# Kernel tuning notes

Hardware: AMD Instinct MI355X
Metric: run time of the kernel (lower is better)

The kernel has to match this reference:

```python
import jax, jax.numpy as jnp
import numpy as np

N = 100_000   # nodes
E = 1_600_000 # edges (avg degree 16)
D = 128       # in_dim
H = 128       # hidden_dim


def _glorot(key, shape):
    s = 1.0 / np.sqrt(shape[0])
    return jax.random.uniform(key, shape, jnp.float32, -s, s)


def setup_inputs() -> dict:
    key = jax.random.key(0)
    ks = jax.random.split(key, 8)
    x = jax.random.normal(ks[0], (N, D), jnp.float32)
    edge_index = jax.random.randint(ks[1], (2, E), 0, N)
    return {
        "x": x,
        "edge_index": edge_index,
        "Wn0": _glorot(ks[2], (D, H)),
        "Wr0": _glorot(ks[3], (D, H)),
        "b0": jnp.zeros((H,), jnp.float32),
        "Wn1": _glorot(ks[4], (H, H)),
        "Wr1": _glorot(ks[5], (H, H)),
        "b1": jnp.zeros((H,), jnp.float32),
        "Wh": _glorot(ks[6], (H, 1)),
        "bh": jnp.zeros((1,), jnp.float32),
    }


def _mean_agg(h, src, dst, n):
    # mean of source-node features scattered onto destination nodes
    summed = jax.ops.segment_sum(h[src], dst, num_segments=n)  # [N, F]
    cnt = jax.ops.segment_sum(jnp.ones((src.shape[0],), h.dtype), dst,
                              num_segments=n)
    return summed / jnp.maximum(cnt, 1.0)[:, None]


def _sage_layer(h, src, dst, Wn, Wr, b):
    # PyG SAGEConv (mean aggr): lin_l(mean_neighbors) + lin_r(root) + bias
    agg = _mean_agg(h, src, dst, h.shape[0])
    return agg @ Wn + h @ Wr + b


def reference(x, edge_index, Wn0, Wr0, b0, Wn1, Wr1, b1, Wh, bh):
    src, dst = edge_index[0], edge_index[1]
    h = jax.nn.relu(_sage_layer(x, src, dst, Wn0, Wr0, b0))  # dropout = identity (eval)
    h = jax.nn.relu(_sage_layer(h, src, dst, Wn1, Wr1, b1))
    logits = (h @ Wh + bh)[:, 0]  # squeeze(-1) -> [N]
    return logits
```

## Files before the change

### kernel.cpp

```cpp
#include <hip/hip_runtime.h>

#define THREADS 256
#define SCAN_ITEMS 8
#define NSB 256
#define BKT_MAX 3200
#define CHUNK 1024

typedef float f32x4 __attribute__((ext_vector_type(4)));
typedef __bf16 bf16x8 __attribute__((ext_vector_type(8)));
typedef int intx4 __attribute__((ext_vector_type(4)));

__device__ inline unsigned short f32_to_bf16_rne(float f) {
    unsigned int u = __float_as_uint(f);
    unsigned int r = u + 0x7fffu + ((u >> 16) & 1u);
    return (unsigned short)(r >> 16);
}
__device__ inline float bf16_bits_to_f32(unsigned short h) {
    return __uint_as_float(((unsigned int)h) << 16);
}
__device__ inline uint4 pack8(const unsigned short* s) {
    uint4 u;
    u.x = (unsigned int)s[0] | ((unsigned int)s[1] << 16);
    u.y = (unsigned int)s[2] | ((unsigned int)s[3] << 16);
    u.z = (unsigned int)s[4] | ((unsigned int)s[5] << 16);
    u.w = (unsigned int)s[6] | ((unsigned int)s[7] << 16);
    return u;
}

__global__ __launch_bounds__(256) void hist32(const int* __restrict__ dst,
                                              int* __restrict__ hist,
                                              int E, int nbkt, int chunk) {
    __shared__ int lh[BKT_MAX];
    const int tid = threadIdx.x, blk = blockIdx.x;
    for (int i = tid; i < nbkt; i += 256) lh[i] = 0;
    __syncthreads();
    int s = blk * chunk, e = s + chunk; if (e > E) e = E;
    if (((size_t)dst & 15) == 0) {
        int n4 = (e > s) ? ((e - s) >> 2) : 0;
        const intx4* d4p = (const intx4*)(dst + s);
        for (int i = tid; i < n4; i += 256) {
            intx4 d4 = d4p[i];
#pragma unroll
            for (int k = 0; k < 4; k++) atomicAdd(&lh[d4[k] >> 5], 1);
        }
        for (int j = s + (n4 << 2) + tid; j < e; j += 256) atomicAdd(&lh[dst[j] >> 5], 1);
    } else {
        for (int j = s + tid; j < e; j += 256) atomicAdd(&lh[dst[j] >> 5], 1);
    }
    __syncthreads();
    for (int i = tid; i < nbkt; i += 256) hist[i * NSB + blk] = lh[i];
}

__global__ void scan1_kernel(const int* __restrict__ cnt, int* __restrict__ off,
                             int* __restrict__ bsums, int n) {
    __shared__ int sdata[THREADS];
    int base = blockIdx.x * (THREADS * SCAN_ITEMS) + threadIdx.x * SCAN_ITEMS;
    int vals[SCAN_ITEMS];
    int tsum = 0;
#pragma unroll
    for (int k = 0; k < SCAN_ITEMS; k++) {
        int idx = base + k;
        int v = (idx < n) ? cnt[idx] : 0;
        vals[k] = tsum;
        tsum += v;
    }
    sdata[threadIdx.x] = tsum;
    __syncthreads();
    for (int s = 1; s < THREADS; s <<= 1) {
        int y = (threadIdx.x >= (unsigned)s) ? sdata[threadIdx.x - s] : 0;
        __syncthreads();
        sdata[threadIdx.x] += y;
        __syncthreads();
    }
    int texcl = sdata[threadIdx.x] - tsum;
#pragma unroll
    for (int k = 0; k < SCAN_ITEMS; k++) {
        int idx = base + k;
        if (idx < n) off[idx] = texcl + vals[k];
    }
    if (threadIdx.x == THREADS - 1) bsums[blockIdx.x] = sdata[THREADS - 1];
}

__global__ void scan2_wave(const int* __restrict__ bsums, int* __restrict__ bbase,
                           int nb, int* __restrict__ offN) {
    const int lane = threadIdx.x;
    int carry = 0;
    for (int base = 0; base < nb; base += 64) {
        int i = base + lane;
        int v = (i < nb) ? bsums[i] : 0;
        int x = v;
#pragma unroll
        for (int s = 1; s < 64; s <<= 1) {
            int y = __shfl_up(x, s);
            if (lane >= s) x += y;
        }
        if (i < nb) bbase[i] = carry + x - v;
        carry += __shfl(x, 63);
    }
    if (lane == 0) *offN = carry;
}

__global__ void scan3b_kernel(int* __restrict__ off, const int* __restrict__ bbase, int n) {
    int i = blockIdx.x * blockDim.x + threadIdx.x;
    if (i < n) off[i] += bbase[i >> 11];
}

__global__ __launch_bounds__(256) void scatter32(const int* __restrict__ src,
                                                 const int* __restrict__ dst,
                                                 const int* __restrict__ hstS,
                                                 int* __restrict__ esrt,
                                                 int E, int nbkt, int chunk) {
    __shared__ int cur[BKT_MAX];
    const int tid = threadIdx.x, blk = blockIdx.x;
    for (int i = tid; i < nbkt; i += 256) cur[i] = hstS[i * NSB + blk];
    __syncthreads();
    int s = blk * chunk, e = s + chunk; if (e > E) e = E;
    if ((((size_t)dst | (size_t)src) & 15) == 0) {
        int n4 = (e > s) ? ((e - s) >> 2) : 0;
        const intx4* d4p = (const intx4*)(dst + s);
        const intx4* s4p = (const intx4*)(src + s);
        for (int i = tid; i < n4; i += 256) {
            intx4 d4 = d4p[i];
            intx4 s4 = s4p[i];
#pragma unroll
            for (int k = 0; k < 4; k++) {
                int d = d4[k];
                int p = atomicAdd(&cur[d >> 5], 1);
                esrt[p] = s4[k] | ((d & 31) << 17);
            }
        }
        for (int j = s + (n4 << 2) + tid; j < e; j += 256) {
            int d = dst[j];
            int p = atomicAdd(&cur[d >> 5], 1);
            esrt[p] = src[j] | ((d & 31) << 17);
        }
    } else {
        for (int j = s + tid; j < e; j += 256) {
            int d = dst[j];
            int p = atomicAdd(&cur[d >> 5], 1);
            esrt[p] = src[j] | ((d & 31) << 17);
        }
    }
}

__global__ void cvt_bf16_kernel(const float4* __restrict__ x, ushort4* __restrict__ o, int n4) {
    int i = blockIdx.x * blockDim.x + threadIdx.x;
    if (i < n4) {
        float4 v = x[i];
        ushort4 r;
        r.x = f32_to_bf16_rne(v.x);
        r.y = f32_to_bf16_rne(v.y);
        r.z = f32_to_bf16_rne(v.z);
        r.w = f32_to_bf16_rne(v.w);
        o[i] = r;
    }
}

__global__ void swizzle_w_kernel(const float* __restrict__ Wn, const float* __restrict__ Wr,
                                 uint4* __restrict__ out) {
    int id = blockIdx.x * blockDim.x + threadIdx.x;
    if (id >= 4096) return;
    int lane = id & 63;
    int nt = (id >> 6) & 7;
    int t = id >> 9;
    int kbase = t * 32 + (lane >> 4) * 8;
    int col = nt * 16 + (lane & 15);
    unsigned short hi[8], lo[8];
#pragma unroll
    for (int j = 0; j < 8; j++) {
        int k = kbase + j;
        const float* W = (k < 128) ? (Wn + (size_t)k * 128) : (Wr + (size_t)(k - 128) * 128);
        float v = W[col];
        unsigned short h = f32_to_bf16_rne(v);
        hi[j] = h;
        lo[j] = f32_to_bf16_rne(v - bf16_bits_to_f32(h));
    }
    out[(size_t)((t * 8 + nt) * 2 + 0) * 64 + lane] = pack8(hi);
    out[(size_t)((t * 8 + nt) * 2 + 1) * 64 + lane] = pack8(lo);
}

__global__ __launch_bounds__(256) void agg_bucket(const unsigned short* __restrict__ hb,
                                                  const int* __restrict__ hstS,
                                                  const int* __restrict__ esrt,
                                                  unsigned short* __restrict__ aggb,
                                                  int E, int nbkt, int n) {
    __shared__ int stage[CHUNK];
    __shared__ int sorted[CHUNK];
    __shared__ int cnt[32];
    __shared__ int coff[33];
    const int tid = threadIdx.x, lane = tid & 63, w = tid >> 6;
    const int b = blockIdx.x;

    const int p0 = hstS[b * NSB];
    const int p1 = (b + 1 < nbkt) ? hstS[(b + 1) * NSB] : E;

    if (p1 - p0 <= CHUNK) {
        int m = p1 - p0;
        for (int i = tid; i < m; i += 256) stage[i] = esrt[p0 + i];
        if (tid < 32) cnt[tid] = 0;
        __syncthreads();
        for (int i = tid; i < m; i += 256) atomicAdd(&cnt[(stage[i] >> 17) & 31], 1);
        __syncthreads();
        if (tid < 32) {
            int v = cnt[tid];
            int x = v;
#pragma unroll
            for (int s = 1; s < 32; s <<= 1) {
                int y = __shfl_up(x, s);
                if (lane >= s) x += y;
            }
            coff[tid + 1] = x;
            if (tid == 0) coff[0] = 0;
            cnt[tid] = x - v;
        }
        __syncthreads();
        for (int i = tid; i < m; i += 256) {
            int pk = stage[i];
            int p = atomicAdd(&cnt[(pk >> 17) & 31], 1);
            sorted[p] = pk;
        }
        __syncthreads();

        int no[9];
#pragma unroll
        for (int i = 0; i <= 8; i++) no[i] = coff[w * 8 + i];
        const int s = no[0], e2 = no[8];
        int curL = 0;
        float ax = 0.f, ay = 0.f;

        auto flushTo = [&](int tgt) {
            while (curL < tgt) {
                int node = b * 32 + w * 8 + curL;
                int d = no[curL + 1] - no[curL];
                float inv = 1.0f / (float)(d > 1 ? d : 1);
                unsigned int o = (unsigned int)f32_to_bf16_rne(ax * inv)
                               | ((unsigned int)f32_to_bf16_rne(ay * inv) << 16);
                if (node < n)
                    *(unsigned int*)(aggb + (size_t)node * 128 + lane * 2) = o;
                ax = 0.f; ay = 0.f; ++curL;
            }
        };
        auto issue = [&](unsigned int* v, int* nd, int base) {
#pragma unroll
            for (int j = 0; j < 8; j++) {
                int pk = sorted[base + j];
                nd[j] = ((pk >> 17) & 31) - w * 8;
                v[j] = *(const unsigned int*)(hb + (size_t)(pk & 0x1FFFF) * 128 + lane * 2);
            }
        };
        auto consume = [&](const unsigned int* v, const int* nd) {
#pragma unroll
            for (int j = 0; j < 8; j++) {
                flushTo(nd[j]);
                ax += __uint_as_float(v[j] << 16);
                ay += __uint_as_float(v[j] & 0xffff0000u);
            }
        };

        const int nb8 = (e2 - s) >> 3;
        unsigned int vA[8], vB[8];
        int ndA[8], ndB[8];
        if (nb8 > 0) {
            issue(vA, ndA, s);
            int k = 1;
            for (; k + 1 < nb8; k += 2) {
                issue(vB, ndB, s + k * 8);
                consume(vA, ndA);
                issue(vA, ndA, s + k * 8 + 8);
                consume(vB, ndB);
            }
            if (k < nb8) {
                issue(vB, ndB, s + k * 8);
                consume(vA, ndA);
                consume(vB, ndB);
            } else {
                consume(vA, ndA);
            }
        }
        for (int i = s + (nb8 << 3); i < e2; i++) {
            int pk = sorted[i];
            flushTo(((pk >> 17) & 31) - w * 8);
            unsigned int vv = *(const unsigned int*)(hb + (size_t)(pk & 0x1FFFF) * 128 + lane * 2);
            ax += __uint_as_float(vv << 16);
            ay += __uint_as_float(vv & 0xffff0000u);
        }
        flushTo(8);
        return;
    }

    float accx[8], accy[8];
    int dcnt[8];
#pragma unroll
    for (int nl = 0; nl < 8; nl++) { accx[nl] = 0.f; accy[nl] = 0.f; dcnt[nl] = 0; }
    for (int base = p0; base < p1; base += CHUNK) {
        int m = p1 - base; if (m > CHUNK) m = CHUNK;
        for (int i = tid; i < m; i += 256) stage[i] = esrt[base + i];
        if (tid < 32) cnt[tid] = 0;
        __syncthreads();
        for (int i = tid; i < m; i += 256) atomicAdd(&cnt[(stage[i] >> 17) & 31], 1);
        __syncthreads();
        if (tid < 32) {
            int v = cnt[tid];
            int x = v;
#pragma unroll
            for (int s = 1; s < 32; s <<= 1) {
                int y = __shfl_up(x, s);
                if (lane >= s) x += y;
            }
            coff[tid + 1] = x;
            if (tid == 0) coff[0] = 0;
            cnt[tid] = x - v;
        }
        __syncthreads();
        for (int i = tid; i < m; i += 256) {
            int pk = stage[i];
            int p = atomicAdd(&cnt[(pk >> 17) & 31], 1);
            sorted[p] = pk;
        }
        __syncthreads();
#pragma unroll
        for (int nl = 0; nl < 8; nl++) {
            int node_l = w * 8 + nl;
            int s = coff[node_l], e2 = coff[node_l + 1];
            dcnt[nl] += e2 - s;
            float ax = accx[nl], ay = accy[nl];
            int i = s;
            for (; i + 8 <= e2; i += 8) {
                unsigned int v[8];
#pragma unroll
                for (int j = 0; j < 8; j++) {
                    int sj = sorted[i + j] & 0x1FFFF;
                    v[j] = *(const unsigned int*)(hb + (size_t)sj * 128 + lane * 2);
                }
#pragma unroll
                for (int j = 0; j < 8; j++) {
                    ax += __uint_as_float(v[j] << 16);
                    ay += __uint_as_float(v[j] & 0xffff0000u);
                }
            }
            for (; i < e2; i++) {
                int sj = sorted[i] & 0x1FFFF;
                unsigned int vv = *(const unsigned int*)(hb + (size_t)sj * 128 + lane * 2);
                ax += __uint_as_float(vv << 16);
                ay += __uint_as_float(vv & 0xffff0000u);
            }
            accx[nl] = ax; accy[nl] = ay;
        }
        __syncthreads();
    }
#pragma unroll
    for (int nl = 0; nl < 8; nl++) {
        int node = b * 32 + w * 8 + nl;
        if (node < n) {
            int d = dcnt[nl];
            float inv = 1.0f / (float)(d > 1 ? d : 1);
            unsigned int o = (unsigned int)f32_to_bf16_rne(accx[nl] * inv)
                           | ((unsigned int)f32_to_bf16_rne(accy[nl] * inv) << 16);
            *(unsigned int*)(aggb + (size_t)node * 128 + lane * 2) = o;
        }
    }
}

template <int LAYER, bool FINAL>
__global__ __launch_bounds__(256, 2) void update_mfma(
    const unsigned short* __restrict__ aggb, const void* __restrict__ hsrc,
    const uint4* __restrict__ Wsw, const float* __restrict__ bias,
    unsigned short* __restrict__ hout,
    const float* __restrict__ Wh, const float* __restrict__ bh,
    float* __restrict__ logits, int n) {
    __shared__ uint4 Alds[2048];
    __shared__ uint4 Wlds[2048];
    const int tid = threadIdx.x;
    const int lane = tid & 63;
    const int w = tid >> 6;
    const int i0 = blockIdx.x * 128;

    f32x4 acc[2][8];
#pragma unroll
    for (int mt = 0; mt < 2; mt++)
#pragma unroll
        for (int nt = 0; nt < 8; nt++) acc[mt][nt] = (f32x4)0.f;

    const int r = tid >> 1;
    const int half = tid & 1;
    const int rg = i0 + r;
    const bool inb = rg < n;
    const int mt_s = r >> 4;
    const int lidx = r & 15;

    for (int c = 0; c < 4; c++) {
        const bool haslo = (LAYER == 0 && c >= 2);
        {
            const uint4* srcW = Wsw + (size_t)c * 2048;
#pragma unroll
            for (int g = 0; g < 8; g++) Wlds[g * 256 + tid] = srcW[g * 256 + tid];
        }
        {
            unsigned short hiA[32], loA[32];
            if (LAYER == 0 && c >= 2) {
                const float4* s4 = (const float4*)((const float*)hsrc + (size_t)rg * 128 +
                                                   (c - 2) * 64 + half * 32);
#pragma unroll
                for (int q = 0; q < 8; q++) {
                    float4 f = inb ? s4[q] : make_float4(0.f, 0.f, 0.f, 0.f);
                    float vv[4] = {f.x, f.y, f.z, f.w};
#pragma unroll
                    for (int e = 0; e < 4; e++) {
                        unsigned short h = f32_to_bf16_rne(vv[e]);
                        hiA[q * 4 + e] = h;
                        loA[q * 4 + e] = f32_to_bf16_rne(vv[e] - bf16_bits_to_f32(h));
                    }
                }
            } else {
                const unsigned short* bsrc = (c < 2) ? aggb : (const unsigned short*)hsrc;
                int cc = (c < 2) ? c : c - 2;
                const uint4* s4 = (const uint4*)(bsrc + (size_t)rg * 128 + cc * 64 + half * 32);
#pragma unroll
                for (int q = 0; q < 4; q++) {
                    uint4 u = inb ? s4[q] : make_uint4(0, 0, 0, 0);
                    unsigned int uu[4] = {u.x, u.y, u.z, u.w};
#pragma unroll
                    for (int e = 0; e < 4; e++) {
                        hiA[q * 8 + e * 2 + 0] = (unsigned short)(uu[e] & 0xffffu);
                        hiA[q * 8 + e * 2 + 1] = (unsigned short)(uu[e] >> 16);
                    }
                }
            }
            unsigned int baseHi = ((mt_s * 2 + half) * 2 + 0) * 64;
#pragma unroll
            for (int g2 = 0; g2 < 4; g2++)
                Alds[baseHi + lidx + 16 * g2] = pack8(&hiA[g2 * 8]);
            if (haslo) {
#pragma unroll
                for (int g2 = 0; g2 < 4; g2++)
                    Alds[baseHi + 64 + lidx + 16 * g2] = pack8(&loA[g2 * 8]);
            }
        }
        __syncthreads();
#pragma unroll
        for (int kt = 0; kt < 2; kt++) {
            bf16x8 a0h = *(const bf16x8*)&Alds[(((w * 2 + 0) * 2 + kt) * 2 + 0) * 64 + lane];
            bf16x8 a1h = *(const bf16x8*)&Alds[(((w * 2 + 1) * 2 + kt) * 2 + 0) * 64 + lane];
            bf16x8 a0l, a1l;
            if (haslo) {
                a0l = *(const bf16x8*)&Alds[(((w * 2 + 0) * 2 + kt) * 2 + 1) * 64 + lane];
                a1l = *(const bf16x8*)&Alds[(((w * 2 + 1) * 2 + kt) * 2 + 1) * 64 + lane];
            }
#pragma unroll
            for (int nt = 0; nt < 8; nt++) {
                bf16x8 bhv = *(const bf16x8*)&Wlds[((kt * 8 + nt) * 2 + 0) * 64 + lane];
                bf16x8 blv = *(const bf16x8*)&Wlds[((kt * 8 + nt) * 2 + 1) * 64 + lane];
                acc[0][nt] = __builtin_amdgcn_mfma_f32_16x16x32_bf16(a0h, bhv, acc[0][nt], 0, 0, 0);
                acc[0][nt] = __builtin_amdgcn_mfma_f32_16x16x32_bf16(a0h, blv, acc[0][nt], 0, 0, 0);
                acc[1][nt] = __builtin_amdgcn_mfma_f32_16x16x32_bf16(a1h, bhv, acc[1][nt], 0, 0, 0);
                acc[1][nt] = __builtin_amdgcn_mfma_f32_16x16x32_bf16(a1h, blv, acc[1][nt], 0, 0, 0);
                if (haslo) {
                    acc[0][nt] = __builtin_amdgcn_mfma_f32_16x16x32_bf16(a0l, bhv, acc[0][nt], 0, 0, 0);
                    acc[1][nt] = __builtin_amdgcn_mfma_f32_16x16x32_bf16(a1l, bhv, acc[1][nt], 0, 0, 0);
                }
            }
        }
        __syncthreads();
    }

    const int col = lane & 15;
    const int g4 = lane >> 4;
    float bcol[8];
#pragma unroll
    for (int nt = 0; nt < 8; nt++) bcol[nt] = bias[nt * 16 + col];
    if (!FINAL) {
#pragma unroll
        for (int mt = 0; mt < 2; mt++) {
            int nodeBase = i0 + (w * 2 + mt) * 16 + g4 * 4;
#pragma unroll
            for (int reg = 0; reg < 4; reg++) {
                int node = nodeBase + reg;
                if (node < n) {
#pragma unroll
                    for (int nt = 0; nt < 8; nt++) {
                        float v = acc[mt][nt][reg] + bcol[nt];
                        v = v > 0.f ? v : 0.f;
                        hout[(size_t)node * 128 + nt * 16 + col] = f32_to_bf16_rne(v);
                    }
                }
            }
        }
    } else {
        float whc[8];
#pragma unroll
        for (int nt = 0; nt < 8; nt++) whc[nt] = Wh[nt * 16 + col];
        float bhv = bh[0];
#pragma unroll
        for (int mt = 0; mt < 2; mt++) {
            int nodeBase = i0 + (w * 2 + mt) * 16 + g4 * 4;
#pragma unroll
            for (int reg = 0; reg < 4; reg++) {
                float s = 0.f;
#pragma unroll
                for (int nt = 0; nt < 8; nt++) {
                    float v = acc[mt][nt][reg] + bcol[nt];
                    v = v > 0.f ? v : 0.f;
                    s += v * whc[nt];
                }
                s += __shfl_xor(s, 1);
                s += __shfl_xor(s, 2);
                s += __shfl_xor(s, 4);
                s += __shfl_xor(s, 8);
                int node = nodeBase + reg;
                if (col == 0 && node < n) logits[node] = s + bhv;
            }
        }
    }
}

extern "C" void kernel_launch(void* const* d_in, const int* in_sizes, int n_in,
                              void* d_out, int out_size, void* d_ws, size_t ws_size,
                              hipStream_t stream) {
    const float* x   = (const float*)d_in[0];
    const int*   ei  = (const int*)d_in[1];
    const float* Wn0 = (const float*)d_in[2];
    const float* Wr0 = (const float*)d_in[3];
    const float* b0  = (const float*)d_in[4];
    const float* Wn1 = (const float*)d_in[5];
    const float* Wr1 = (const float*)d_in[6];
    const float* b1  = (const float*)d_in[7];
    const float* Wh  = (const float*)d_in[8];
    const float* bh  = (const float*)d_in[9];
    float* logits = (float*)d_out;

    int N = in_sizes[0] / 128;
    int E = in_sizes[1] / 2;
    const int* src = ei;
    const int* dst = ei + E;

    int nbkt = (N + 31) >> 5;
    int HS = nbkt * NSB;
    int NB = (HS + 2047) / 2048;
    int chunk = (((E + NSB - 1) / NSB) + 3) & ~3;

    char* ws = (char*)d_ws;
    size_t cur = 0;
    auto alloc = [&](size_t bytes) -> void* {
        void* p = ws + cur;
        cur += (bytes + 255) & ~(size_t)255;
        return p;
    };
    int* hist  = (int*)alloc((size_t)HS * 4);
    int* bsums = (int*)alloc((size_t)NB * 4);
    int* bbase = (int*)alloc((size_t)NB * 4);
    int* scrat = (int*)alloc(256);
    int* esrt  = (int*)alloc((size_t)E * 4);
    unsigned short* xb  = (unsigned short*)alloc((size_t)N * 128 * 2);
    unsigned short* h0b = (unsigned short*)alloc((size_t)N * 128 * 2);
    unsigned short* agb = (unsigned short*)alloc((size_t)N * 128 * 2);
    uint4* Wsw0 = (uint4*)alloc(131072);
    uint4* Wsw1 = (uint4*)alloc(131072);
    (void)ws_size; (void)n_in; (void)out_size;

    int n4 = N * 32;
    hipLaunchKernelGGL(cvt_bf16_kernel, dim3((n4 + 255) / 256), dim3(256), 0, stream,
                       (const float4*)x, (ushort4*)xb, n4);
    hipLaunchKernelGGL(swizzle_w_kernel, dim3(16), dim3(256), 0, stream, Wn0, Wr0, Wsw0);
    hipLaunchKernelGGL(swizzle_w_kernel, dim3(16), dim3(256), 0, stream, Wn1, Wr1, Wsw1);

    hipLaunchKernelGGL(hist32,        dim3(NSB), dim3(256), 0, stream, dst, hist, E, nbkt, chunk);
    hipLaunchKernelGGL(scan1_kernel,  dim3(NB),  dim3(256), 0, stream, hist, hist, bsums, HS);
    hipLaunchKernelGGL(scan2_wave,    dim3(1),   dim3(64),  0, stream, bsums, bbase, NB, scrat);
    hipLaunchKernelGGL(scan3b_kernel, dim3((HS + 255) / 256), dim3(256), 0, stream, hist, bbase, HS);
    hipLaunchKernelGGL(scatter32,     dim3(NSB), dim3(256), 0, stream, src, dst, hist, esrt, E, nbkt, chunk);

    int gUpd = (N + 127) / 128;

    hipLaunchKernelGGL(agg_bucket, dim3(nbkt), dim3(256), 0, stream, xb, hist, esrt, agb, E, nbkt, N);
    hipLaunchKernelGGL((update_mfma<0, false>), dim3(gUpd), dim3(256), 0, stream,
                       agb, (const void*)x, Wsw0, b0, h0b, nullptr, nullptr, nullptr, N);
    hipLaunchKernelGGL(agg_bucket, dim3(nbkt), dim3(256), 0, stream, h0b, hist, esrt, agb, E, nbkt, N);
    hipLaunchKernelGGL((update_mfma<1, true>), dim3(gUpd), dim3(256), 0, stream,
                       agb, (const void*)h0b, Wsw1, b1, nullptr, Wh, bh, logits, N);
}
```

Measured before the change: 362.2 us.

## Fuse prep kernels, halve sort blocks, and gather two edges per wave with 8-byte loads

Merges the histogram, bf16 conversion and both weight-swizzle kernels into one launch, and halves the number of histogram/scatter blocks (NSB). The packed edge key now stores the source index pre-shifted by 8 bits, so a mask yields the byte offset of the row directly. The aggregation fast path splits each wave into two halves that each fetch a different edge's row as 8-byte loads and combine their sums with a cross-half shuffle. The aim is fewer launches and more gather loads in flight, at the cost of extra shuffles and divergent handling when paired edges target different nodes.

```diff
diff --git a/kernel.cpp b/kernel.cpp
--- a/kernel.cpp
+++ b/kernel.cpp
@@ -2,11 +2,12 @@
 
 #define THREADS 256
 #define SCAN_ITEMS 8
-#define NSB 256
+#define NSB 128
 #define BKT_MAX 3200
 #define CHUNK 1024
 
 typedef float f32x4 __attribute__((ext_vector_type(4)));
+typedef float floatx2 __attribute__((ext_vector_type(2)));
 typedef __bf16 bf16x8 __attribute__((ext_vector_type(8)));
 typedef int intx4 __attribute__((ext_vector_type(4)));
 
@@ -27,28 +28,62 @@
     return u;
 }
 
-__global__ __launch_bounds__(256) void hist32(const int* __restrict__ dst,
-                                              int* __restrict__ hist,
-                                              int E, int nbkt, int chunk) {
+__global__ __launch_bounds__(256) void prep(
+    const int* __restrict__ dst, int* __restrict__ hist, int E, int nbkt, int chunk,
+    const float4* __restrict__ x4, ushort4* __restrict__ xb4, int n4,
+    const float* __restrict__ Wn0, const float* __restrict__ Wr0, uint4* __restrict__ Wsw0,
+    const float* __restrict__ Wn1, const float* __restrict__ Wr1, uint4* __restrict__ Wsw1) {
     __shared__ int lh[BKT_MAX];
     const int tid = threadIdx.x, blk = blockIdx.x;
-    for (int i = tid; i < nbkt; i += 256) lh[i] = 0;
-    __syncthreads();
-    int s = blk * chunk, e = s + chunk; if (e > E) e = E;
-    if (((size_t)dst & 15) == 0) {
-        int n4 = (e > s) ? ((e - s) >> 2) : 0;
+    if (blk < NSB) {
+        for (int i = tid; i < nbkt; i += 256) lh[i] = 0;
+        __syncthreads();
+        int s = blk * chunk, e = s + chunk; if (e > E) e = E;
+        int n4e = (e > s) ? ((e - s) >> 2) : 0;
         const intx4* d4p = (const intx4*)(dst + s);
-        for (int i = tid; i < n4; i += 256) {
+        for (int i = tid; i < n4e; i += 256) {
             intx4 d4 = d4p[i];
 #pragma unroll
             for (int k = 0; k < 4; k++) atomicAdd(&lh[d4[k] >> 5], 1);
         }
-        for (int j = s + (n4 << 2) + tid; j < e; j += 256) atomicAdd(&lh[dst[j] >> 5], 1);
+        for (int j = s + (n4e << 2) + tid; j < e; j += 256) atomicAdd(&lh[dst[j] >> 5], 1);
+        __syncthreads();
+        for (int i = tid; i < nbkt; i += 256) hist[i * NSB + blk] = lh[i];
+    } else if (blk < NSB + 32) {
+        int b2 = blk - NSB;
+        const float* Wn = (b2 < 16) ? Wn0 : Wn1;
+        const float* Wr = (b2 < 16) ? Wr0 : Wr1;
+        uint4* out = (b2 < 16) ? Wsw0 : Wsw1;
+        int id = (b2 & 15) * 256 + tid;
+        int lane = id & 63;
+        int nt = (id >> 6) & 7;
+        int t = id >> 9;
+        int kbase = t * 32 + (lane >> 4) * 8;
+        int col = nt * 16 + (lane & 15);
+        unsigned short hi[8], lo[8];
+#pragma unroll
+        for (int j = 0; j < 8; j++) {
+            int k = kbase + j;
+            const float* W = (k < 128) ? (Wn + (size_t)k * 128) : (Wr + (size_t)(k - 128) * 128);
+            float v = W[col];
+            unsigned short h = f32_to_bf16_rne(v);
+            hi[j] = h;
+            lo[j] = f32_to_bf16_rne(v - bf16_bits_to_f32(h));
+        }
+        out[(size_t)((t * 8 + nt) * 2 + 0) * 64 + lane] = pack8(hi);
+        out[(size_t)((t * 8 + nt) * 2 + 1) * 64 + lane] = pack8(lo);
     } else {
-        for (int j = s + tid; j < e; j += 256) atomicAdd(&lh[dst[j] >> 5], 1);
-    }
-    __syncthreads();
-    for (int i = tid; i < nbkt; i += 256) hist[i * NSB + blk] = lh[i];
+        int i = (blk - NSB - 32) * 256 + tid;
+        if (i < n4) {
+            float4 v = x4[i];
+            ushort4 r;
+            r.x = f32_to_bf16_rne(v.x);
+            r.y = f32_to_bf16_rne(v.y);
+            r.z = f32_to_bf16_rne(v.z);
+            r.w = f32_to_bf16_rne(v.w);
+            xb4[i] = r;
+        }
+    }
 }
 
 __global__ void scan1_kernel(const int* __restrict__ cnt, int* __restrict__ off,
@@ -126,57 +161,21 @@
             for (int k = 0; k < 4; k++) {
                 int d = d4[k];
                 int p = atomicAdd(&cur[d >> 5], 1);
-                esrt[p] = s4[k] | ((d & 31) << 17);
+                esrt[p] = (s4[k] << 8) | ((d & 31) << 25);
             }
         }
         for (int j = s + (n4 << 2) + tid; j < e; j += 256) {
             int d = dst[j];
             int p = atomicAdd(&cur[d >> 5], 1);
-            esrt[p] = src[j] | ((d & 31) << 17);
+            esrt[p] = (src[j] << 8) | ((d & 31) << 25);
         }
     } else {
         for (int j = s + tid; j < e; j += 256) {
             int d = dst[j];
             int p = atomicAdd(&cur[d >> 5], 1);
-            esrt[p] = src[j] | ((d & 31) << 17);
-        }
-    }
-}
-
-__global__ void cvt_bf16_kernel(const float4* __restrict__ x, ushort4* __restrict__ o, int n4) {
-    int i = blockIdx.x * blockDim.x + threadIdx.x;
-    if (i < n4) {
-        float4 v = x[i];
-        ushort4 r;
-        r.x = f32_to_bf16_rne(v.x);
-        r.y = f32_to_bf16_rne(v.y);
-        r.z = f32_to_bf16_rne(v.z);
-        r.w = f32_to_bf16_rne(v.w);
-        o[i] = r;
-    }
-}
-
-__global__ void swizzle_w_kernel(const float* __restrict__ Wn, const float* __restrict__ Wr,
-                                 uint4* __restrict__ out) {
-    int id = blockIdx.x * blockDim.x + threadIdx.x;
-    if (id >= 4096) return;
-    int lane = id & 63;
-    int nt = (id >> 6) & 7;
-    int t = id >> 9;
-    int kbase = t * 32 + (lane >> 4) * 8;
-    int col = nt * 16 + (lane & 15);
-    unsigned short hi[8], lo[8];
-#pragma unroll
-    for (int j = 0; j < 8; j++) {
-        int k = kbase + j;
-        const float* W = (k < 128) ? (Wn + (size_t)k * 128) : (Wr + (size_t)(k - 128) * 128);
-        float v = W[col];
-        unsigned short h = f32_to_bf16_rne(v);
-        hi[j] = h;
-        lo[j] = f32_to_bf16_rne(v - bf16_bits_to_f32(h));
-    }
-    out[(size_t)((t * 8 + nt) * 2 + 0) * 64 + lane] = pack8(hi);
-    out[(size_t)((t * 8 + nt) * 2 + 1) * 64 + lane] = pack8(lo);
+            esrt[p] = (src[j] << 8) | ((d & 31) << 25);
+        }
+    }
 }
 
 __global__ __launch_bounds__(256) void agg_bucket(const unsigned short* __restrict__ hb,
@@ -199,7 +198,7 @@
         for (int i = tid; i < m; i += 256) stage[i] = esrt[p0 + i];
         if (tid < 32) cnt[tid] = 0;
         __syncthreads();
-        for (int i = tid; i < m; i += 256) atomicAdd(&cnt[(stage[i] >> 17) & 31], 1);
+        for (int i = tid; i < m; i += 256) atomicAdd(&cnt[(stage[i] >> 25) & 31], 1);
         __syncthreads();
         if (tid < 32) {
             int v = cnt[tid];
@@ -216,73 +215,100 @@
         __syncthreads();
         for (int i = tid; i < m; i += 256) {
             int pk = stage[i];
-            int p = atomicAdd(&cnt[(pk >> 17) & 31], 1);
+            int p = atomicAdd(&cnt[(pk >> 25) & 31], 1);
             sorted[p] = pk;
         }
         __syncthreads();
 
-        int no[9];
-#pragma unroll
-        for (int i = 0; i <= 8; i++) no[i] = coff[w * 8 + i];
-        const int s = no[0], e2 = no[8];
+        const int w8 = w * 8;
+        const int s = __builtin_amdgcn_readfirstlane(coff[w8]);
+        const int e2 = __builtin_amdgcn_readfirstlane(coff[w8 + 8]);
+        const char* hbB = (const char*)hb;
+        const unsigned laneOff = (unsigned)(lane & 31) * 8u;
+        const bool hiH = lane >= 32;
+        floatx2 a01 = (floatx2)0.f, a23 = (floatx2)0.f;
         int curL = 0;
-        float ax = 0.f, ay = 0.f;
 
         auto flushTo = [&](int tgt) {
             while (curL < tgt) {
-                int node = b * 32 + w * 8 + curL;
-                int d = no[curL + 1] - no[curL];
+                float t0 = a01.x + __shfl_xor(a01.x, 32);
+                float t1 = a01.y + __shfl_xor(a01.y, 32);
+                float t2 = a23.x + __shfl_xor(a23.x, 32);
+                float t3 = a23.y + __shfl_xor(a23.y, 32);
+                int node = b * 32 + w8 + curL;
+                int d = coff[w8 + curL + 1] - coff[w8 + curL];
                 float inv = 1.0f / (float)(d > 1 ? d : 1);
-                unsigned int o = (unsigned int)f32_to_bf16_rne(ax * inv)
-                               | ((unsigned int)f32_to_bf16_rne(ay * inv) << 16);
-                if (node < n)
-                    *(unsigned int*)(aggb + (size_t)node * 128 + lane * 2) = o;
-                ax = 0.f; ay = 0.f; ++curL;
+                if (!hiH && node < n) {
+                    uint2 o;
+                    o.x = (unsigned int)f32_to_bf16_rne(t0 * inv)
+                        | ((unsigned int)f32_to_bf16_rne(t1 * inv) << 16);
+                    o.y = (unsigned int)f32_to_bf16_rne(t2 * inv)
+                        | ((unsigned int)f32_to_bf16_rne(t3 * inv) << 16);
+                    *(uint2*)((char*)aggb + (size_t)node * 256 + laneOff) = o;
+                }
+                a01 = (floatx2)0.f; a23 = (floatx2)0.f;
+                ++curL;
             }
         };
-        auto issue = [&](unsigned int* v, int* nd, int base) {
-#pragma unroll
-            for (int j = 0; j < 8; j++) {
-                int pk = sorted[base + j];
-                nd[j] = ((pk >> 17) & 31) - w * 8;
-                v[j] = *(const unsigned int*)(hb + (size_t)(pk & 0x1FFFF) * 128 + lane * 2);
-            }
+        auto accum = [&](uint2 v) {
+            floatx2 p0v = { __uint_as_float(v.x << 16), __uint_as_float(v.x & 0xffff0000u) };
+            floatx2 p1v = { __uint_as_float(v.y << 16), __uint_as_float(v.y & 0xffff0000u) };
+            a01 += p0v; a23 += p1v;
         };
-        auto consume = [&](const unsigned int* v, const int* nd) {
-#pragma unroll
-            for (int j = 0; j < 8; j++) {
-                flushTo(nd[j]);
-                ax += __uint_as_float(v[j] << 16);
-                ay += __uint_as_float(v[j] & 0xffff0000u);
+        auto issueB = [&](uint2* v, int* ke, int* ko, int base) {
+#pragma unroll
+            for (int j = 0; j < 4; j++) {
+                int kEv = sorted[base + 2 * j];
+                int kOv = sorted[base + 2 * j + 1];
+                ke[j] = __builtin_amdgcn_readfirstlane(kEv);
+                ko[j] = __builtin_amdgcn_readfirstlane(kOv);
+                int kSel = hiH ? kOv : kEv;
+                unsigned off = (unsigned)(kSel & 0x01FFFF00) + laneOff;
+                v[j] = *(const uint2*)(hbB + off);
             }
         };
+        auto consumeB = [&](const uint2* v, const int* ke, const int* ko) {
+#pragma unroll
+            for (int j = 0; j < 4; j++) {
+                int nE = (ke[j] >> 25) - w8;
+                int nO = (ko[j] >> 25) - w8;
+                if (nE == nO) {
+                    flushTo(nE);
+                    accum(v[j]);
+                } else {
+                    flushTo(nE);
+                    if (!hiH) accum(v[j]);
+                    flushTo(nO);
+                    if (hiH) accum(v[j]);
+                }
+            }
+        };
 
         const int nb8 = (e2 - s) >> 3;
-        unsigned int vA[8], vB[8];
-        int ndA[8], ndB[8];
+        uint2 vA[4], vB[4];
+        int keA[4], koA[4], keB[4], koB[4];
         if (nb8 > 0) {
-            issue(vA, ndA, s);
+            issueB(vA, keA, koA, s);
             int k = 1;
             for (; k + 1 < nb8; k += 2) {
-                issue(vB, ndB, s + k * 8);
-                consume(vA, ndA);
-                issue(vA, ndA, s + k * 8 + 8);
-                consume(vB, ndB);
+                issueB(vB, keB, koB, s + k * 8);
+                consumeB(vA, keA, koA);
+                issueB(vA, keA, koA, s + k * 8 + 8);
+                consumeB(vB, keB, koB);
             }
             if (k < nb8) {
-                issue(vB, ndB, s + k * 8);
-                consume(vA, ndA);
-                consume(vB, ndB);
+                issueB(vB, keB, koB, s + k * 8);
+                consumeB(vA, keA, koA);
+                consumeB(vB, keB, koB);
             } else {
-                consume(vA, ndA);
+                consumeB(vA, keA, koA);
             }
         }
         for (int i = s + (nb8 << 3); i < e2; i++) {
-            int pk = sorted[i];
-            flushTo(((pk >> 17) & 31) - w * 8);
-            unsigned int vv = *(const unsigned int*)(hb + (size_t)(pk & 0x1FFFF) * 128 + lane * 2);
-            ax += __uint_as_float(vv << 16);
-            ay += __uint_as_float(vv & 0xffff0000u);
+            int ks = __builtin_amdgcn_readfirstlane(sorted[i]);
+            flushTo((ks >> 25) - w8);
+            uint2 vv = *(const uint2*)(hbB + (unsigned)(ks & 0x01FFFF00) + laneOff);
+            if (!hiH) accum(vv);
         }
         flushTo(8);
         return;
@@ -297,7 +323,7 @@
         for (int i = tid; i < m; i += 256) stage[i] = esrt[base + i];
         if (tid < 32) cnt[tid] = 0;
         __syncthreads();
-        for (int i = tid; i < m; i += 256) atomicAdd(&cnt[(stage[i] >> 17) & 31], 1);
+        for (int i = tid; i < m; i += 256) atomicAdd(&cnt[(stage[i] >> 25) & 31], 1);
         __syncthreads();
         if (tid < 32) {
             int v = cnt[tid];
@@ -314,7 +340,7 @@
         __syncthreads();
         for (int i = tid; i < m; i += 256) {
             int pk = stage[i];
-            int p = atomicAdd(&cnt[(pk >> 17) & 31], 1);
+            int p = atomicAdd(&cnt[(pk >> 25) & 31], 1);
             sorted[p] = pk;
         }
         __syncthreads();
@@ -329,8 +355,8 @@
                 unsigned int v[8];
 #pragma unroll
                 for (int j = 0; j < 8; j++) {
-                    int sj = sorted[i + j] & 0x1FFFF;
-                    v[j] = *(const unsigned int*)(hb + (size_t)sj * 128 + lane * 2);
+                    unsigned off = (unsigned)(sorted[i + j] & 0x01FFFF00);
+                    v[j] = *(const unsigned int*)((const char*)hb + off + lane * 4);
                 }
 #pragma unroll
                 for (int j = 0; j < 8; j++) {
@@ -339,8 +365,8 @@
                 }
             }
             for (; i < e2; i++) {
-                int sj = sorted[i] & 0x1FFFF;
-                unsigned int vv = *(const unsigned int*)(hb + (size_t)sj * 128 + lane * 2);
+                unsigned off = (unsigned)(sorted[i] & 0x01FFFF00);
+                unsigned int vv = *(const unsigned int*)((const char*)hb + off + lane * 4);
                 ax += __uint_as_float(vv << 16);
                 ay += __uint_as_float(vv & 0xffff0000u);
             }
@@ -558,12 +584,12 @@
     (void)ws_size; (void)n_in; (void)out_size;
 
     int n4 = N * 32;
-    hipLaunchKernelGGL(cvt_bf16_kernel, dim3((n4 + 255) / 256), dim3(256), 0, stream,
-                       (const float4*)x, (ushort4*)xb, n4);
-    hipLaunchKernelGGL(swizzle_w_kernel, dim3(16), dim3(256), 0, stream, Wn0, Wr0, Wsw0);
-    hipLaunchKernelGGL(swizzle_w_kernel, dim3(16), dim3(256), 0, stream, Wn1, Wr1, Wsw1);
-
-    hipLaunchKernelGGL(hist32,        dim3(NSB), dim3(256), 0, stream, dst, hist, E, nbkt, chunk);
+    int gPrep = NSB + 32 + (n4 + 255) / 256;
+    hipLaunchKernelGGL(prep, dim3(gPrep), dim3(256), 0, stream,
+                       dst, hist, E, nbkt, chunk,
+                       (const float4*)x, (ushort4*)xb, n4,
+                       Wn0, Wr0, Wsw0, Wn1, Wr1, Wsw1);
+
     hipLaunchKernelGGL(scan1_kernel,  dim3(NB),  dim3(256), 0, stream, hist, hist, bsums, HS);
     hipLaunchKernelGGL(scan2_wave,    dim3(1),   dim3(64),  0, stream, bsums, bbase, NB, scrat);
     hipLaunchKernelGGL(scan3b_kernel, dim3((HS + 255) / 256), dim3(256), 0, stream, hist, bbase, HS);
```

New measurement: 345.7 us. -4.6%, faster.

## Merge prep kernels, fold scan fixup into consumers, read weights directly from global

Applied to the files above, without the earlier changes.

Merges the bf16 conversion, both weight swizzles and the histogram into one prep launch, and halves the number of histogram sub-blocks. The block-base scan fixup kernel is removed: scatter and aggregation now add bbase themselves. Packed edge entries are pre-shifted so source offsets become byte offsets with no multiply. The update kernel no longer stages weights in LDS and reads them from global or L2 instead. Launch count and LDS use drop, at the cost of more global weight reads inside the MFMA loop and fewer histogram blocks running in parallel.

```diff
diff --git a/kernel.cpp b/kernel.cpp
--- a/kernel.cpp
+++ b/kernel.cpp
@@ -2,7 +2,7 @@
 
 #define THREADS 256
 #define SCAN_ITEMS 8
-#define NSB 256
+#define NSB 128
 #define BKT_MAX 3200
 #define CHUNK 1024
 
@@ -27,28 +27,62 @@
     return u;
 }
 
-__global__ __launch_bounds__(256) void hist32(const int* __restrict__ dst,
-                                              int* __restrict__ hist,
-                                              int E, int nbkt, int chunk) {
+__global__ __launch_bounds__(256) void prep(
+    const int* __restrict__ dst, int* __restrict__ hist, int E, int nbkt, int chunk,
+    const float4* __restrict__ x4, ushort4* __restrict__ xb4, int n4,
+    const float* __restrict__ Wn0, const float* __restrict__ Wr0, uint4* __restrict__ Wsw0,
+    const float* __restrict__ Wn1, const float* __restrict__ Wr1, uint4* __restrict__ Wsw1) {
     __shared__ int lh[BKT_MAX];
     const int tid = threadIdx.x, blk = blockIdx.x;
-    for (int i = tid; i < nbkt; i += 256) lh[i] = 0;
-    __syncthreads();
-    int s = blk * chunk, e = s + chunk; if (e > E) e = E;
-    if (((size_t)dst & 15) == 0) {
-        int n4 = (e > s) ? ((e - s) >> 2) : 0;
+    if (blk < NSB) {
+        for (int i = tid; i < nbkt; i += 256) lh[i] = 0;
+        __syncthreads();
+        int s = blk * chunk, e = s + chunk; if (e > E) e = E;
+        int n4e = (e > s) ? ((e - s) >> 2) : 0;
         const intx4* d4p = (const intx4*)(dst + s);
-        for (int i = tid; i < n4; i += 256) {
+        for (int i = tid; i < n4e; i += 256) {
             intx4 d4 = d4p[i];
 #pragma unroll
             for (int k = 0; k < 4; k++) atomicAdd(&lh[d4[k] >> 5], 1);
         }
-        for (int j = s + (n4 << 2) + tid; j < e; j += 256) atomicAdd(&lh[dst[j] >> 5], 1);
+        for (int j = s + (n4e << 2) + tid; j < e; j += 256) atomicAdd(&lh[dst[j] >> 5], 1);
+        __syncthreads();
+        for (int i = tid; i < nbkt; i += 256) hist[i * NSB + blk] = lh[i];
+    } else if (blk < NSB + 32) {
+        int b2 = blk - NSB;
+        const float* Wn = (b2 < 16) ? Wn0 : Wn1;
+        const float* Wr = (b2 < 16) ? Wr0 : Wr1;
+        uint4* out = (b2 < 16) ? Wsw0 : Wsw1;
+        int id = (b2 & 15) * 256 + tid;
+        int lane = id & 63;
+        int nt = (id >> 6) & 7;
+        int t = id >> 9;
+        int kbase = t * 32 + (lane >> 4) * 8;
+        int col = nt * 16 + (lane & 15);
+        unsigned short hi[8], lo[8];
+#pragma unroll
+        for (int j = 0; j < 8; j++) {
+            int k = kbase + j;
+            const float* W = (k < 128) ? (Wn + (size_t)k * 128) : (Wr + (size_t)(k - 128) * 128);
+            float v = W[col];
+            unsigned short h = f32_to_bf16_rne(v);
+            hi[j] = h;
+            lo[j] = f32_to_bf16_rne(v - bf16_bits_to_f32(h));
+        }
+        out[(size_t)((t * 8 + nt) * 2 + 0) * 64 + lane] = pack8(hi);
+        out[(size_t)((t * 8 + nt) * 2 + 1) * 64 + lane] = pack8(lo);
     } else {
-        for (int j = s + tid; j < e; j += 256) atomicAdd(&lh[dst[j] >> 5], 1);
-    }
-    __syncthreads();
-    for (int i = tid; i < nbkt; i += 256) hist[i * NSB + blk] = lh[i];
+        int i = (blk - NSB - 32) * 256 + tid;
+        if (i < n4) {
+            float4 v = x4[i];
+            ushort4 r;
+            r.x = f32_to_bf16_rne(v.x);
+            r.y = f32_to_bf16_rne(v.y);
+            r.z = f32_to_bf16_rne(v.z);
+            r.w = f32_to_bf16_rne(v.w);
+            xb4[i] = r;
+        }
+    }
 }
 
 __global__ void scan1_kernel(const int* __restrict__ cnt, int* __restrict__ off,
@@ -100,19 +134,18 @@
     if (lane == 0) *offN = carry;
 }
 
-__global__ void scan3b_kernel(int* __restrict__ off, const int* __restrict__ bbase, int n) {
-    int i = blockIdx.x * blockDim.x + threadIdx.x;
-    if (i < n) off[i] += bbase[i >> 11];
-}
-
 __global__ __launch_bounds__(256) void scatter32(const int* __restrict__ src,
                                                  const int* __restrict__ dst,
                                                  const int* __restrict__ hstS,
+                                                 const int* __restrict__ bbase,
                                                  int* __restrict__ esrt,
                                                  int E, int nbkt, int chunk) {
     __shared__ int cur[BKT_MAX];
     const int tid = threadIdx.x, blk = blockIdx.x;
-    for (int i = tid; i < nbkt; i += 256) cur[i] = hstS[i * NSB + blk];
+    for (int i = tid; i < nbkt; i += 256) {
+        int j = i * NSB + blk;
+        cur[i] = hstS[j] + bbase[j >> 11];
+    }
     __syncthreads();
     int s = blk * chunk, e = s + chunk; if (e > E) e = E;
     if ((((size_t)dst | (size_t)src) & 15) == 0) {
@@ -126,61 +159,26 @@
             for (int k = 0; k < 4; k++) {
                 int d = d4[k];
                 int p = atomicAdd(&cur[d >> 5], 1);
-                esrt[p] = s4[k] | ((d & 31) << 17);
+                esrt[p] = (s4[k] << 8) | ((d & 31) << 25);
             }
         }
         for (int j = s + (n4 << 2) + tid; j < e; j += 256) {
             int d = dst[j];
             int p = atomicAdd(&cur[d >> 5], 1);
-            esrt[p] = src[j] | ((d & 31) << 17);
+            esrt[p] = (src[j] << 8) | ((d & 31) << 25);
         }
     } else {
         for (int j = s + tid; j < e; j += 256) {
             int d = dst[j];
             int p = atomicAdd(&cur[d >> 5], 1);
-            esrt[p] = src[j] | ((d & 31) << 17);
-        }
-    }
-}
-
-__global__ void cvt_bf16_kernel(const float4* __restrict__ x, ushort4* __restrict__ o, int n4) {
-    int i = blockIdx.x * blockDim.x + threadIdx.x;
-    if (i < n4) {
-        float4 v = x[i];
-        ushort4 r;
-        r.x = f32_to_bf16_rne(v.x);
-        r.y = f32_to_bf16_rne(v.y);
-        r.z = f32_to_bf16_rne(v.z);
-        r.w = f32_to_bf16_rne(v.w);
-        o[i] = r;
-    }
-}
-
-__global__ void swizzle_w_kernel(const float* __restrict__ Wn, const float* __restrict__ Wr,
-                                 uint4* __restrict__ out) {
-    int id = blockIdx.x * blockDim.x + threadIdx.x;
-    if (id >= 4096) return;
-    int lane = id & 63;
-    int nt = (id >> 6) & 7;
-    int t = id >> 9;
-    int kbase = t * 32 + (lane >> 4) * 8;
-    int col = nt * 16 + (lane & 15);
-    unsigned short hi[8], lo[8];
-#pragma unroll
-    for (int j = 0; j < 8; j++) {
-        int k = kbase + j;
-        const float* W = (k < 128) ? (Wn + (size_t)k * 128) : (Wr + (size_t)(k - 128) * 128);
-        float v = W[col];
-        unsigned short h = f32_to_bf16_rne(v);
-        hi[j] = h;
-        lo[j] = f32_to_bf16_rne(v - bf16_bits_to_f32(h));
-    }
-    out[(size_t)((t * 8 + nt) * 2 + 0) * 64 + lane] = pack8(hi);
-    out[(size_t)((t * 8 + nt) * 2 + 1) * 64 + lane] = pack8(lo);
+            esrt[p] = (src[j] << 8) | ((d & 31) << 25);
+        }
+    }
 }
 
 __global__ __launch_bounds__(256) void agg_bucket(const unsigned short* __restrict__ hb,
                                                   const int* __restrict__ hstS,
+                                                  const int* __restrict__ bbase,
                                                   const int* __restrict__ esrt,
                                                   unsigned short* __restrict__ aggb,
                                                   int E, int nbkt, int n) {
@@ -191,15 +189,21 @@
     const int tid = threadIdx.x, lane = tid & 63, w = tid >> 6;
     const int b = blockIdx.x;
 
-    const int p0 = hstS[b * NSB];
-    const int p1 = (b + 1 < nbkt) ? hstS[(b + 1) * NSB] : E;
+    int j0 = b * NSB;
+    const int p0 = hstS[j0] + bbase[j0 >> 11];
+    int p1 = E;
+    if (b + 1 < nbkt) {
+        int j1 = (b + 1) * NSB;
+        p1 = hstS[j1] + bbase[j1 >> 11];
+    }
+    const char* hbB = (const char*)hb;
 
     if (p1 - p0 <= CHUNK) {
         int m = p1 - p0;
         for (int i = tid; i < m; i += 256) stage[i] = esrt[p0 + i];
         if (tid < 32) cnt[tid] = 0;
         __syncthreads();
-        for (int i = tid; i < m; i += 256) atomicAdd(&cnt[(stage[i] >> 17) & 31], 1);
+        for (int i = tid; i < m; i += 256) atomicAdd(&cnt[stage[i] >> 25], 1);
         __syncthreads();
         if (tid < 32) {
             int v = cnt[tid];
@@ -216,7 +220,7 @@
         __syncthreads();
         for (int i = tid; i < m; i += 256) {
             int pk = stage[i];
-            int p = atomicAdd(&cnt[(pk >> 17) & 31], 1);
+            int p = atomicAdd(&cnt[pk >> 25], 1);
             sorted[p] = pk;
         }
         __syncthreads();
@@ -225,18 +229,19 @@
 #pragma unroll
         for (int i = 0; i <= 8; i++) no[i] = coff[w * 8 + i];
         const int s = no[0], e2 = no[8];
+        const int w8 = w * 8;
         int curL = 0;
         float ax = 0.f, ay = 0.f;
 
         auto flushTo = [&](int tgt) {
             while (curL < tgt) {
-                int node = b * 32 + w * 8 + curL;
+                int node = b * 32 + w8 + curL;
                 int d = no[curL + 1] - no[curL];
                 float inv = 1.0f / (float)(d > 1 ? d : 1);
                 unsigned int o = (unsigned int)f32_to_bf16_rne(ax * inv)
                                | ((unsigned int)f32_to_bf16_rne(ay * inv) << 16);
                 if (node < n)
-                    *(unsigned int*)(aggb + (size_t)node * 128 + lane * 2) = o;
+                    *(unsigned int*)((char*)aggb + (size_t)node * 256 + lane * 4) = o;
                 ax = 0.f; ay = 0.f; ++curL;
             }
         };
@@ -244,8 +249,8 @@
 #pragma unroll
             for (int j = 0; j < 8; j++) {
                 int pk = sorted[base + j];
-                nd[j] = ((pk >> 17) & 31) - w * 8;
-                v[j] = *(const unsigned int*)(hb + (size_t)(pk & 0x1FFFF) * 128 + lane * 2);
+                nd[j] = (pk >> 25) - w8;
+                v[j] = *(const unsigned int*)(hbB + (unsigned)(pk & 0x01FFFF00) + lane * 4);
             }
         };
         auto consume = [&](const unsigned int* v, const int* nd) {
@@ -279,8 +284,8 @@
         }
         for (int i = s + (nb8 << 3); i < e2; i++) {
             int pk = sorted[i];
-            flushTo(((pk >> 17) & 31) - w * 8);
-            unsigned int vv = *(const unsigned int*)(hb + (size_t)(pk & 0x1FFFF) * 128 + lane * 2);
+            flushTo((pk >> 25) - w8);
+            unsigned int vv = *(const unsigned int*)(hbB + (unsigned)(pk & 0x01FFFF00) + lane * 4);
             ax += __uint_as_float(vv << 16);
             ay += __uint_as_float(vv & 0xffff0000u);
         }
@@ -297,7 +302,7 @@
         for (int i = tid; i < m; i += 256) stage[i] = esrt[base + i];
         if (tid < 32) cnt[tid] = 0;
         __syncthreads();
-        for (int i = tid; i < m; i += 256) atomicAdd(&cnt[(stage[i] >> 17) & 31], 1);
+        for (int i = tid; i < m; i += 256) atomicAdd(&cnt[stage[i] >> 25], 1);
         __syncthreads();
         if (tid < 32) {
             int v = cnt[tid];
@@ -314,7 +319,7 @@
         __syncthreads();
         for (int i = tid; i < m; i += 256) {
             int pk = stage[i];
-            int p = atomicAdd(&cnt[(pk >> 17) & 31], 1);
+            int p = atomicAdd(&cnt[pk >> 25], 1);
             sorted[p] = pk;
         }
         __syncthreads();
@@ -329,8 +334,8 @@
                 unsigned int v[8];
 #pragma unroll
                 for (int j = 0; j < 8; j++) {
-                    int sj = sorted[i + j] & 0x1FFFF;
-                    v[j] = *(const unsigned int*)(hb + (size_t)sj * 128 + lane * 2);
+                    unsigned off = (unsigned)(sorted[i + j] & 0x01FFFF00);
+                    v[j] = *(const unsigned int*)(hbB + off + lane * 4);
                 }
 #pragma unroll
                 for (int j = 0; j < 8; j++) {
@@ -339,8 +344,8 @@
                 }
             }
             for (; i < e2; i++) {
-                int sj = sorted[i] & 0x1FFFF;
-                unsigned int vv = *(const unsigned int*)(hb + (size_t)sj * 128 + lane * 2);
+                unsigned off = (unsigned)(sorted[i] & 0x01FFFF00);
+                unsigned int vv = *(const unsigned int*)(hbB + off + lane * 4);
                 ax += __uint_as_float(vv << 16);
                 ay += __uint_as_float(vv & 0xffff0000u);
             }
@@ -369,7 +374,6 @@
     const float* __restrict__ Wh, const float* __restrict__ bh,
     float* __restrict__ logits, int n) {
     __shared__ uint4 Alds[2048];
-    __shared__ uint4 Wlds[2048];
     const int tid = threadIdx.x;
     const int lane = tid & 63;
     const int w = tid >> 6;
@@ -391,11 +395,6 @@
     for (int c = 0; c < 4; c++) {
         const bool haslo = (LAYER == 0 && c >= 2);
         {
-            const uint4* srcW = Wsw + (size_t)c * 2048;
-#pragma unroll
-            for (int g = 0; g < 8; g++) Wlds[g * 256 + tid] = srcW[g * 256 + tid];
-        }
-        {
             unsigned short hiA[32], loA[32];
             if (LAYER == 0 && c >= 2) {
                 const float4* s4 = (const float4*)((const float*)hsrc + (size_t)rg * 128 +
@@ -437,6 +436,7 @@
             }
         }
         __syncthreads();
+        const uint4* Wc = Wsw + (size_t)c * 2048;
 #pragma unroll
         for (int kt = 0; kt < 2; kt++) {
             bf16x8 a0h = *(const bf16x8*)&Alds[(((w * 2 + 0) * 2 + kt) * 2 + 0) * 64 + lane];
@@ -448,8 +448,8 @@
             }
 #pragma unroll
             for (int nt = 0; nt < 8; nt++) {
-                bf16x8 bhv = *(const bf16x8*)&Wlds[((kt * 8 + nt) * 2 + 0) * 64 + lane];
-                bf16x8 blv = *(const bf16x8*)&Wlds[((kt * 8 + nt) * 2 + 1) * 64 + lane];
+                bf16x8 bhv = *(const bf16x8*)&Wc[((kt * 8 + nt) * 2 + 0) * 64 + lane];
+                bf16x8 blv = *(const bf16x8*)&Wc[((kt * 8 + nt) * 2 + 1) * 64 + lane];
                 acc[0][nt] = __builtin_amdgcn_mfma_f32_16x16x32_bf16(a0h, bhv, acc[0][nt], 0, 0, 0);
                 acc[0][nt] = __builtin_amdgcn_mfma_f32_16x16x32_bf16(a0h, blv, acc[0][nt], 0, 0, 0);
                 acc[1][nt] = __builtin_amdgcn_mfma_f32_16x16x32_bf16(a1h, bhv, acc[1][nt], 0, 0, 0);
@@ -558,23 +558,22 @@
     (void)ws_size; (void)n_in; (void)out_size;
 
     int n4 = N * 32;
-    hipLaunchKernelGGL(cvt_bf16_kernel, dim3((n4 + 255) / 256), dim3(256), 0, stream,
-                       (const float4*)x, (ushort4*)xb, n4);
-    hipLaunchKernelGGL(swizzle_w_kernel, dim3(16), dim3(256), 0, stream, Wn0, Wr0, Wsw0);
-    hipLaunchKernelGGL(swizzle_w_kernel, dim3(16), dim3(256), 0, stream, Wn1, Wr1, Wsw1);
-
-    hipLaunchKernelGGL(hist32,        dim3(NSB), dim3(256), 0, stream, dst, hist, E, nbkt, chunk);
+    int gPrep = NSB + 32 + (n4 + 255) / 256;
+    hipLaunchKernelGGL(prep, dim3(gPrep), dim3(256), 0, stream,
+                       dst, hist, E, nbkt, chunk,
+                       (const float4*)x, (ushort4*)xb, n4,
+                       Wn0, Wr0, Wsw0, Wn1, Wr1, Wsw1);
+
     hipLaunchKernelGGL(scan1_kernel,  dim3(NB),  dim3(256), 0, stream, hist, hist, bsums, HS);
     hipLaunchKernelGGL(scan2_wave,    dim3(1),   dim3(64),  0, stream, bsums, bbase, NB, scrat);
-    hipLaunchKernelGGL(scan3b_kernel, dim3((HS + 255) / 256), dim3(256), 0, stream, hist, bbase, HS);
-    hipLaunchKernelGGL(scatter32,     dim3(NSB), dim3(256), 0, stream, src, dst, hist, esrt, E, nbkt, chunk);
+    hipLaunchKernelGGL(scatter32,     dim3(NSB), dim3(256), 0, stream, src, dst, hist, bbase, esrt, E, nbkt, chunk);
 
     int gUpd = (N + 127) / 128;
 
-    hipLaunchKernelGGL(agg_bucket, dim3(nbkt), dim3(256), 0, stream, xb, hist, esrt, agb, E, nbkt, N);
+    hipLaunchKernelGGL(agg_bucket, dim3(nbkt), dim3(256), 0, stream, xb, hist, bbase, esrt, agb, E, nbkt, N);
     hipLaunchKernelGGL((update_mfma<0, false>), dim3(gUpd), dim3(256), 0, stream,
                        agb, (const void*)x, Wsw0, b0, h0b, nullptr, nullptr, nullptr, N);
-    hipLaunchKernelGGL(agg_bucket, dim3(nbkt), dim3(256), 0, stream, h0b, hist, esrt, agb, E, nbkt, N);
+    hipLaunchKernelGGL(agg_bucket, dim3(nbkt), dim3(256), 0, stream, h0b, hist, bbase, esrt, agb, E, nbkt, N);
     hipLaunchKernelGGL((update_mfma<1, true>), dim3(gUpd), dim3(256), 0, stream,
                        agb, (const void*)h0b, Wsw1, b1, nullptr, Wh, bh, logits, N);
 }
```

Result: slower. 385.4 us (+6.4%).
